# Kernel optimization log

Measured on AMD Instinct MI355X. Metric: run time of the kernel, lower is better.

The kernel has to match this reference:

```python
import jax, jax.numpy as jnp
import numpy as np

B, T, SD = 16, 512, 64          # batch, action seq len, sample_dim
EMB, HD = 1024, 64              # emb_dim, head_dim
NH = EMB // HD                  # 16 heads
DEPTH, NREG, LAT, FF = 8, 16, 256, 4 * EMB
S = T + NREG                    # total sequence length (actions + registers)


def setup_inputs() -> dict:
    key = jax.random.key(0)
    ks = jax.random.split(key, 16)
    def n(k, shape, scale=0.02):
        return jax.random.normal(k, shape, jnp.float32) * scale
    return {
        "sample": jax.random.normal(ks[0], (B, T, SD), jnp.float32),
        "W_emb": n(ks[1], (SD, EMB)), "b_emb": jnp.zeros((EMB,), jnp.float32),
        "pos": n(ks[2], (T, EMB)),
        "registers": n(ks[3], (NREG, EMB), 1.0),
        "ln1_s": jnp.ones((DEPTH, EMB), jnp.float32), "ln1_b": jnp.zeros((DEPTH, EMB), jnp.float32),
        "W_qkv": n(ks[4], (DEPTH, EMB, 3 * EMB)), "b_qkv": jnp.zeros((DEPTH, 3 * EMB), jnp.float32),
        "W_o": n(ks[5], (DEPTH, EMB, EMB)), "b_o": jnp.zeros((DEPTH, EMB), jnp.float32),
        "ln2_s": jnp.ones((DEPTH, EMB), jnp.float32), "ln2_b": jnp.zeros((DEPTH, EMB), jnp.float32),
        "W_fc1": n(ks[6], (DEPTH, EMB, FF)), "b_fc1": jnp.zeros((DEPTH, FF), jnp.float32),
        "W_fc2": n(ks[7], (DEPTH, FF, EMB)), "b_fc2": jnp.zeros((DEPTH, EMB), jnp.float32),
        "lnf_s": jnp.ones((EMB,), jnp.float32), "lnf_b": jnp.zeros((EMB,), jnp.float32),
        "W_head": n(ks[8], (EMB, LAT)), "b_head": jnp.zeros((LAT,), jnp.float32),
    }


def _ln(x, s, b):
    m = jnp.mean(x, -1, keepdims=True)
    v = jnp.var(x, -1, keepdims=True)
    return (x - m) * jax.lax.rsqrt(v + 1e-5) * s + b


def _causal_last_mask():
    # True = attended to. Actions attend to all actions but NOT registers;
    # registers attend to all actions and causally (incl. self) to registers.
    allowed = jnp.ones((S, S), jnp.bool_)
    allowed = allowed.at[:T, T:].set(False)
    allowed = allowed.at[T:, T:].set(jnp.tril(jnp.ones((NREG, NREG), jnp.bool_)))
    return allowed


def reference(sample, W_emb, b_emb, pos, registers, ln1_s, ln1_b, W_qkv, b_qkv,
              W_o, b_o, ln2_s, ln2_b, W_fc1, b_fc1, W_fc2, b_fc2,
              lnf_s, lnf_b, W_head, b_head):
    # embed + positional add
    x = sample @ W_emb + b_emb + pos[None, :, :]          # [B,T,E]
    # concat registers
    x = jnp.concatenate([x, jnp.broadcast_to(registers, (B, NREG, EMB))], axis=1)  # [B,S,E]
    mask = _causal_last_mask()                             # [S,S]
    scale = 1.0 / jnp.sqrt(jnp.asarray(HD, x.dtype))
    for i in range(DEPTH):
        # pre-LN multi-head attention with structured block mask
        h = _ln(x, ln1_s[i], ln1_b[i])
        qkv = h @ W_qkv[i] + b_qkv[i]
        q, k, v = jnp.split(qkv, 3, axis=-1)
        q = q.reshape(B, S, NH, HD)
        k = k.reshape(B, S, NH, HD)
        v = v.reshape(B, S, NH, HD)
        att = jnp.einsum('bqhd,bkhd->bhqk', q, k) * scale
        att = jnp.where(mask[None, None], att, jnp.finfo(att.dtype).min)
        att = jax.nn.softmax(att, axis=-1)
        o = jnp.einsum('bhqk,bkhd->bqhd', att, v).reshape(B, S, EMB)
        x = x + o @ W_o[i] + b_o[i]
        # pre-LN MLP
        h2 = _ln(x, ln2_s[i], ln2_b[i])
        x = x + jax.nn.gelu(h2 @ W_fc1[i] + b_fc1[i]) @ W_fc2[i] + b_fc2[i]
    x = _ln(x, lnf_s, lnf_b)
    # head applied to register positions only
    return x[:, T:] @ W_head + b_head                      # [B,NREG,LAT]
```

## Files before the change

### kernel.cpp

```cpp
#include <hip/hip_runtime.h>
#include <hip/hip_bf16.h>


typedef unsigned short u16;
typedef __attribute__((ext_vector_type(4))) float f32x4;
typedef __attribute__((ext_vector_type(8))) __bf16 bf16x8;

#define DEV static __device__ __forceinline__

constexpr int Bb = 16, Tt = 512, E = 1024, HD = 64, NHd = 16;
constexpr int DEPTH = 8, NREG = 16, LAT = 256, FF = 4096;
constexpr int S = Tt + NREG;
constexpr int SPAD = 576;
constexpr int MR = Bb * S;
constexpr int ME = Bb * Tt;

DEV u16 f2bf(float f) {
  unsigned u = __builtin_bit_cast(unsigned, f);
  u += 0x7fffu + ((u >> 16) & 1u);
  return (u16)(u >> 16);
}

DEV void gll16(const u16* g, u16* l) {
  __builtin_amdgcn_global_load_lds((const __attribute__((address_space(1))) void*)g,
                                   (__attribute__((address_space(3))) void*)l, 16, 0, 0);
}

enum { M_EMBED, M_QKV, M_OPROJ, M_FC1, M_FC2, M_HEAD };

struct GA {
  const u16* A; const u16* Bt;
  int K, lda, ldb, Nrows, ldc;
  const float* bias; const float* pos;
  float* fout; u16* bout;
  u16 *qp, *kp, *vtp;
};

template<int MODE, int BN>
__global__ __launch_bounds__(256)
void gemm_bt(GA g) {
  constexpr int NI = BN / 32;
  __shared__ __align__(16) u16 As[3][128 * 32];
  __shared__ __align__(16) u16 Bs[3][BN * 32];
  const int tid = threadIdx.x;
  const u16* A  = g.A;
  const u16* Bt = g.Bt;

  int tM, tN;
  {
    const int nwg = gridDim.x * gridDim.y;
    int flat = blockIdx.y * gridDim.x + blockIdx.x;
    const int q = nwg >> 3, r = nwg & 7;
    const int xcd = flat & 7, loc = flat >> 3;
    flat = (xcd < r ? xcd * (q + 1) : r * (q + 1) + (xcd - r) * q) + loc;
    tM = flat / gridDim.x; tN = flat % gridDim.x;
  }

  const int lane = tid & 63, wid = tid >> 6;
  const int wr = wid >> 1, wc = wid & 1;
  const int fr = lane & 15, fg = lane >> 4;

  const int arow = tM * 128 + (tid >> 2);
  int br0 = tN * BN + (tid >> 2);
  if (br0 > g.Nrows - 1) br0 = g.Nrows - 1;
  int br1 = tN * BN + 64 + (tid >> 2);
  if (br1 > g.Nrows - 1) br1 = g.Nrows - 1;
  const int kseg = ((tid & 3) ^ ((tid >> 3) & 3)) * 8;
  const int woff = (tid & 192) * 8;

  const u16* ag0 = A  + (long)arow        * g.lda + kseg;
  const u16* ag1 = A  + (long)(arow + 64) * g.lda + kseg;
  const u16* bg0 = Bt + (long)br0         * g.ldb + kseg;
  const u16* bg1 = Bt + (long)br1         * g.ldb + kseg;

  f32x4 acc[4][NI];
#pragma unroll
  for (int i = 0; i < 4; ++i)
#pragma unroll
    for (int j = 0; j < NI; ++j) acc[i][j] = f32x4{0.f, 0.f, 0.f, 0.f};

#define STAGE(KT, BUF) do {                                   \
    const int _k0 = (KT) << 5;                                \
    gll16(ag0 + _k0, &As[BUF][woff]);                         \
    gll16(ag1 + _k0, &As[BUF][woff + 2048]);                  \
    gll16(bg0 + _k0, &Bs[BUF][woff]);                         \
    if (BN == 128) gll16(bg1 + _k0, &Bs[BUF][woff + 2048]);   \
  } while (0)

  const int nk = g.K >> 5;
  STAGE(0, 0);
  if (nk > 1) STAGE(1, 1);

  const int rsw = (fg ^ ((fr >> 1) & 3)) * 8;
  constexpr int LPS = (BN == 128) ? 4 : 3;

  for (int kt = 0; kt < nk; ++kt) {
    const int cur = kt % 3;
    if (kt < nk - 1) {
      asm volatile("s_waitcnt vmcnt(%0)" :: "i"(LPS) : "memory");
    } else {
      asm volatile("s_waitcnt vmcnt(0)" ::: "memory");
    }
    __builtin_amdgcn_sched_barrier(0);
    __builtin_amdgcn_s_barrier();
    __builtin_amdgcn_sched_barrier(0);
    if (kt + 2 < nk) STAGE(kt + 2, (kt + 2) % 3);

    bf16x8 af[4], bfr[NI];
#pragma unroll
    for (int mi = 0; mi < 4; ++mi)
      af[mi] = *(const bf16x8*)&As[cur][(wr * 64 + mi * 16 + fr) * 32 + rsw];
#pragma unroll
    for (int ni = 0; ni < NI; ++ni)
      bfr[ni] = *(const bf16x8*)&Bs[cur][(wc * (BN / 2) + ni * 16 + fr) * 32 + rsw];
    __builtin_amdgcn_s_setprio(1);
#pragma unroll
    for (int mi = 0; mi < 4; ++mi)
#pragma unroll
      for (int ni = 0; ni < NI; ++ni)
        acc[mi][ni] = __builtin_amdgcn_mfma_f32_16x16x32_bf16(af[mi], bfr[ni], acc[mi][ni], 0, 0, 0);
    __builtin_amdgcn_s_setprio(0);
  }
#undef STAGE

#pragma unroll
  for (int mi = 0; mi < 4; ++mi)
#pragma unroll
    for (int ni = 0; ni < NI; ++ni)
#pragma unroll
      for (int j = 0; j < 4; ++j) {
        const int row = tM * 128 + wr * 64 + mi * 16 + fg * 4 + j;
        const int col = tN * BN + wc * (BN / 2) + ni * 16 + fr;
        float v = acc[mi][ni][j];
        if (MODE == M_EMBED) {
          const int b = row >> 9, t = row & 511;
          v += g.bias[col] + g.pos[(long)t * E + col];
          g.fout[((long)(b * S + t)) * E + col] = v;
        } else if (MODE == M_QKV) {
          const int b = row / S, s = row - b * S;
          v += g.bias[col];
          const int part = col >> 10, c = col & 1023;
          const int hh = c >> 6, d = c & 63;
          const u16 bf = f2bf(v);
          if (part == 0)      g.qp [((long)((b * NHd + hh) * SPAD + s)) * HD + d] = bf;
          else if (part == 1) g.kp [((long)((b * NHd + hh) * SPAD + s)) * HD + d] = bf;
          else                g.vtp[((long)((b * NHd + hh) * HD   + d)) * SPAD + s] = bf;
        } else if (MODE == M_OPROJ || MODE == M_FC2) {
          const long idx = (long)row * g.ldc + col;
          g.fout[idx] += v + g.bias[col];
        } else if (MODE == M_FC1) {
          v += g.bias[col];
          const float z = 0.7978845608028654f * (v + 0.044715f * v * v * v);
          const float e = __expf(2.f * z);
          const float th = 1.f - 2.f / (e + 1.f);
          g.bout[(long)row * g.ldc + col] = f2bf(0.5f * v * (1.f + th));
        } else if (MODE == M_HEAD) {
          g.fout[(long)row * g.ldc + col] = v + g.bias[col];
        }
      }
}

__global__ __launch_bounds__(256)
void flash_k(const u16* __restrict__ q, const u16* __restrict__ k,
             const u16* __restrict__ vt, u16* __restrict__ o) {
  __shared__ __align__(16) u16 Ks[2][64 * 64];
  __shared__ __align__(16) u16 Vs[2][64 * 64];
  __shared__ __align__(16) u16 Ps[4 * 16 * 64];
  const int tid = threadIdx.x;
  const int lane = tid & 63, w = tid >> 6;
  const int fr = lane & 15, fg = lane >> 4;

  int flat = blockIdx.y * 9 + blockIdx.x;
  flat = (flat & 7) * 288 + (flat >> 3);
  const int bh = flat / 9, qt = flat % 9;
  const int q0 = qt * 64;

  const u16* qrow = q + ((long)bh * SPAD + q0 + w * 16 + fr) * HD;
  const bf16x8 qf0 = *(const bf16x8*)(qrow + fg * 8);
  const bf16x8 qf1 = *(const bf16x8*)(qrow + 32 + fg * 8);

  const int srow = lane >> 3;
  const int sseg = (((lane & 7) ^ (srow & 7)) * 8);
  const u16* kg = k  + ((long)bh * SPAD + w * 16 + srow) * HD + sseg;
  const u16* vg = vt + ((long)(bh * HD + w * 16 + srow)) * SPAD + sseg;

#define STAGE_F(KT, BUF) do {                                       \
    gll16(kg + (KT) * 64 * HD,          &Ks[BUF][w * 16 * HD]);     \
    gll16(kg + (KT) * 64 * HD + 8 * HD, &Ks[BUF][w * 16 * HD + 8 * HD]); \
    gll16(vg + (KT) * 64,               &Vs[BUF][w * 16 * HD]);     \
    gll16(vg + (KT) * 64 + 8 * SPAD,    &Vs[BUF][w * 16 * HD + 8 * HD]); \
  } while (0)

  const int frm = fr & 7;

  float m[4], lsum[4]; f32x4 oa[4];
#pragma unroll
  for (int j = 0; j < 4; ++j) { m[j] = -1e30f; lsum[j] = 0.f; }
#pragma unroll
  for (int n = 0; n < 4; ++n) oa[n] = f32x4{0.f, 0.f, 0.f, 0.f};

  const int nt = (q0 < Tt) ? 8 : 9;
  STAGE_F(0, 0);
  for (int kt = 0; kt < nt; ++kt) {
    const int cur = kt & 1;
    asm volatile("s_waitcnt vmcnt(0)" ::: "memory");
    __builtin_amdgcn_sched_barrier(0);
    __builtin_amdgcn_s_barrier();
    __builtin_amdgcn_sched_barrier(0);
    if (kt + 1 < nt) STAGE_F(kt + 1, cur ^ 1);

    f32x4 sfr[4];
#pragma unroll
    for (int n = 0; n < 4; ++n) {
      const bf16x8 kf0 = *(const bf16x8*)&Ks[cur][(n * 16 + fr) * HD + ((fg ^ frm) * 8)];
      const bf16x8 kf1 = *(const bf16x8*)&Ks[cur][(n * 16 + fr) * HD + (((fg + 4) ^ frm) * 8)];
      sfr[n] = __builtin_amdgcn_mfma_f32_16x16x32_bf16(qf0, kf0, f32x4{0.f,0.f,0.f,0.f}, 0, 0, 0);
      sfr[n] = __builtin_amdgcn_mfma_f32_16x16x32_bf16(qf1, kf1, sfr[n], 0, 0, 0);
    }
    float p[4][4];
#pragma unroll
    for (int j = 0; j < 4; ++j) {
      const int qg = q0 + w * 16 + fg * 4 + j;
      const int vlim = qg < Tt ? Tt : qg + 1;
#pragma unroll
      for (int n = 0; n < 4; ++n) {
        const int col = kt * 64 + n * 16 + fr;
        p[n][j] = (col < vlim) ? sfr[n][j] * 0.125f : -1e30f;
      }
    }
#pragma unroll
    for (int j = 0; j < 4; ++j) {
      float pm = fmaxf(fmaxf(p[0][j], p[1][j]), fmaxf(p[2][j], p[3][j]));
#pragma unroll
      for (int msk = 1; msk <= 8; msk <<= 1) pm = fmaxf(pm, __shfl_xor(pm, msk));
      const float mn = fmaxf(m[j], pm);
      const float corr = __expf(m[j] - mn);
      m[j] = mn;
      float rs = 0.f;
#pragma unroll
      for (int n = 0; n < 4; ++n) { const float e = __expf(p[n][j] - mn); p[n][j] = e; rs += e; }
#pragma unroll
      for (int msk = 1; msk <= 8; msk <<= 1) rs += __shfl_xor(rs, msk);
      lsum[j] = lsum[j] * corr + rs;
#pragma unroll
      for (int n = 0; n < 4; ++n) oa[n][j] *= corr;
    }
#pragma unroll
    for (int j = 0; j < 4; ++j) {
      const int r = fg * 4 + j;
#pragma unroll
      for (int n = 0; n < 4; ++n) {
        const int gr = 2 * n + (fr >> 3);
        Ps[w * 1024 + r * 64 + ((gr ^ (r & 7)) * 8) + frm] = f2bf(p[n][j]);
      }
    }
    asm volatile("s_waitcnt lgkmcnt(0)" ::: "memory");
    __builtin_amdgcn_sched_barrier(0);
    const bf16x8 pf0 = *(const bf16x8*)&Ps[w * 1024 + fr * 64 + ((fg ^ frm) * 8)];
    const bf16x8 pf1 = *(const bf16x8*)&Ps[w * 1024 + fr * 64 + (((fg + 4) ^ frm) * 8)];
#pragma unroll
    for (int n = 0; n < 4; ++n) {
      const bf16x8 vf0 = *(const bf16x8*)&Vs[cur][(n * 16 + fr) * HD + ((fg ^ frm) * 8)];
      const bf16x8 vf1 = *(const bf16x8*)&Vs[cur][(n * 16 + fr) * HD + (((fg + 4) ^ frm) * 8)];
      oa[n] = __builtin_amdgcn_mfma_f32_16x16x32_bf16(pf0, vf0, oa[n], 0, 0, 0);
      oa[n] = __builtin_amdgcn_mfma_f32_16x16x32_bf16(pf1, vf1, oa[n], 0, 0, 0);
    }
  }
#undef STAGE_F

  const int b = bh >> 4, hh = bh & 15;
#pragma unroll
  for (int j = 0; j < 4; ++j) {
    const int qg = q0 + w * 16 + fg * 4 + j;
    if (qg < S) {
      const float inv = 1.f / lsum[j];
#pragma unroll
      for (int n = 0; n < 4; ++n)
        o[((long)(b * S + qg)) * E + hh * HD + n * 16 + fr] = f2bf(oa[n][j] * inv);
    }
  }
}

__global__ __launch_bounds__(256)
void ln_k(const float* __restrict__ x, const float* __restrict__ sc,
          const float* __restrict__ bi, u16* __restrict__ out, int gather) {
  const int r = blockIdx.x;
  const int srow = gather ? ((r >> 4) * S + Tt + (r & 15)) : r;
  const float4 v = ((const float4*)(x + (long)srow * E))[threadIdx.x];
  float s = v.x + v.y + v.z + v.w;
  float q = v.x * v.x + v.y * v.y + v.z * v.z + v.w * v.w;
#pragma unroll
  for (int o = 32; o; o >>= 1) { s += __shfl_down(s, o); q += __shfl_down(q, o); }
  __shared__ float ps[8];
  if ((threadIdx.x & 63) == 0) { ps[threadIdx.x >> 6] = s; ps[4 + (threadIdx.x >> 6)] = q; }
  __syncthreads();
  s = ps[0] + ps[1] + ps[2] + ps[3];
  q = ps[4] + ps[5] + ps[6] + ps[7];
  const float mean = s * (1.f / E);
  const float rs = rsqrtf(q * (1.f / E) - mean * mean + 1e-5f);
  const int c = threadIdx.x * 4;
  ushort4 o4;
  o4.x = f2bf((v.x - mean) * rs * sc[c + 0] + bi[c + 0]);
  o4.y = f2bf((v.y - mean) * rs * sc[c + 1] + bi[c + 1]);
  o4.z = f2bf((v.z - mean) * rs * sc[c + 2] + bi[c + 2]);
  o4.w = f2bf((v.w - mean) * rs * sc[c + 3] + bi[c + 3]);
  ((ushort4*)(out + (long)r * E))[threadIdx.x] = o4;
}

__global__ __launch_bounds__(256)
void wtrans(const float* __restrict__ src, u16* __restrict__ dst, int R, int C) {
  __shared__ float t[32][33];
  const int c0 = blockIdx.x * 32, r0 = blockIdx.y * 32;
  const int tx = threadIdx.x & 31, ty = threadIdx.x >> 5;
#pragma unroll
  for (int i = 0; i < 32; i += 8) t[ty + i][tx] = src[(long)(r0 + ty + i) * C + c0 + tx];
  __syncthreads();
#pragma unroll
  for (int i = 0; i < 32; i += 8) dst[(long)(c0 + ty + i) * R + r0 + tx] = f2bf(t[tx][ty + i]);
}

__global__ void cvt_bf(const float* __restrict__ in, u16* __restrict__ out, long n) {
  const long i = ((long)blockIdx.x * blockDim.x + threadIdx.x) * 4;
  if (i >= n) return;
  const float4 v = *(const float4*)(in + i);
  ushort4 o; o.x = f2bf(v.x); o.y = f2bf(v.y); o.z = f2bf(v.z); o.w = f2bf(v.w);
  *(ushort4*)(out + i) = o;
}

__global__ void zero_k(float4* p, long n) {
  long i = (long)blockIdx.x * blockDim.x + threadIdx.x;
  const long st = (long)gridDim.x * blockDim.x;
  const float4 z = make_float4(0.f, 0.f, 0.f, 0.f);
  for (; i < n; i += st) p[i] = z;
}

__global__ void reg_copy(const float* __restrict__ regs, float* __restrict__ x) {
  const int b = blockIdx.x >> 4, r = blockIdx.x & 15;
  const float4* sp = (const float4*)(regs + (long)r * E);
  float4* dp = (float4*)(x + ((long)(b * S + Tt + r)) * E);
  dp[threadIdx.x] = sp[threadIdx.x];
}

constexpr long OFF_WQKV = 0L;
constexpr long OFF_WO   = OFF_WQKV + 3072L * 1024 * 2;
constexpr long OFF_WFC1 = OFF_WO   + 1024L * 1024 * 2;
constexpr long OFF_WFC2 = OFF_WFC1 + 4096L * 1024 * 2;
constexpr long OFF_WEMB = OFF_WFC2 + 1024L * 4096 * 2;
constexpr long OFF_WHEAD= OFF_WEMB + 1024L * 64 * 2;
constexpr long OFF_SMP  = OFF_WHEAD+ 256L * 1024 * 2;
constexpr long OFF_X    = OFF_SMP  + (long)ME * 64 * 2;
constexpr long OFF_H    = OFF_X    + (long)MR * E * 4;
constexpr long OFF_Q    = OFF_H    + (long)MR * E * 2;
constexpr long OFF_K    = OFF_Q    + 256L * SPAD * HD * 2;
constexpr long OFF_VT   = OFF_K    + 256L * SPAD * HD * 2;
constexpr long OFF_O    = OFF_VT   + 256L * SPAD * HD * 2;
constexpr long OFF_HF   = OFF_O    + (long)MR * FF * 2;
constexpr long WS_NEED  = OFF_HF   + 256L * 1024 * 2;

extern "C" void kernel_launch(void* const* d_in, const int* in_sizes, int n_in,
                              void* d_out, int out_size, void* d_ws, size_t ws_size,
                              hipStream_t stream) {
  if (ws_size < (size_t)WS_NEED) return;

  const float* sample = (const float*)d_in[0];
  const float* W_emb  = (const float*)d_in[1];
  const float* b_emb  = (const float*)d_in[2];
  const float* pos    = (const float*)d_in[3];
  const float* regs   = (const float*)d_in[4];
  const float* ln1_s  = (const float*)d_in[5];
  const float* ln1_b  = (const float*)d_in[6];
  const float* W_qkv  = (const float*)d_in[7];
  const float* b_qkv  = (const float*)d_in[8];
  const float* W_o    = (const float*)d_in[9];
  const float* b_o    = (const float*)d_in[10];
  const float* ln2_s  = (const float*)d_in[11];
  const float* ln2_b  = (const float*)d_in[12];
  const float* W_fc1  = (const float*)d_in[13];
  const float* b_fc1  = (const float*)d_in[14];
  const float* W_fc2  = (const float*)d_in[15];
  const float* b_fc2  = (const float*)d_in[16];
  const float* lnf_s  = (const float*)d_in[17];
  const float* lnf_b  = (const float*)d_in[18];
  const float* W_head = (const float*)d_in[19];
  const float* b_head = (const float*)d_in[20];

  char* w = (char*)d_ws;
  u16* wqkvT = (u16*)(w + OFF_WQKV);
  u16* woT   = (u16*)(w + OFF_WO);
  u16* wfc1T = (u16*)(w + OFF_WFC1);
  u16* wfc2T = (u16*)(w + OFF_WFC2);
  u16* wembT = (u16*)(w + OFF_WEMB);
  u16* wheadT= (u16*)(w + OFF_WHEAD);
  u16* smp   = (u16*)(w + OFF_SMP);
  float* x   = (float*)(w + OFF_X);
  u16* h     = (u16*)(w + OFF_H);
  u16* qp    = (u16*)(w + OFF_Q);
  u16* kp    = (u16*)(w + OFF_K);
  u16* vtp   = (u16*)(w + OFF_VT);
  u16* o     = (u16*)(w + OFF_O);
  u16* a1    = (u16*)(w + OFF_O);
  u16* hf    = (u16*)(w + OFF_HF);

  wtrans<<<dim3(32, 2, 1), 256, 0, stream>>>(W_emb,  wembT, 64, 1024);
  wtrans<<<dim3(8, 32, 1), 256, 0, stream>>>(W_head, wheadT, 1024, 256);
  cvt_bf<<<dim3(512), 256, 0, stream>>>(sample, smp, (long)ME * 64);
  zero_k<<<dim3(2048), 256, 0, stream>>>((float4*)qp, (3L * 256 * SPAD * HD * 2) / 16);

  {
    GA g{}; g.A = smp; g.Bt = wembT; g.K = 64; g.lda = 64; g.ldb = 64;
    g.Nrows = E; g.bias = b_emb; g.pos = pos; g.fout = x;
    gemm_bt<M_EMBED, 64><<<dim3(16, 64, 1), 256, 0, stream>>>(g);
  }
  reg_copy<<<dim3(256), 256, 0, stream>>>(regs, x);

  for (int L = 0; L < DEPTH; ++L) {
    wtrans<<<dim3(96, 32, 1),  256, 0, stream>>>(W_qkv + (long)L * 1024 * 3072, wqkvT, 1024, 3072);
    wtrans<<<dim3(32, 32, 1),  256, 0, stream>>>(W_o   + (long)L * 1024 * 1024, woT,   1024, 1024);
    wtrans<<<dim3(128, 32, 1), 256, 0, stream>>>(W_fc1 + (long)L * 1024 * 4096, wfc1T, 1024, 4096);
    wtrans<<<dim3(32, 128, 1), 256, 0, stream>>>(W_fc2 + (long)L * 4096 * 1024, wfc2T, 4096, 1024);

    ln_k<<<dim3(MR), 256, 0, stream>>>(x, ln1_s + L * E, ln1_b + L * E, h, 0);
    {
      GA g{}; g.A = h; g.Bt = wqkvT;
      g.K = 1024; g.lda = 1024; g.ldb = 1024; g.Nrows = 3072;
      g.bias = b_qkv + L * 3072; g.qp = qp; g.kp = kp; g.vtp = vtp;
      gemm_bt<M_QKV, 128><<<dim3(24, 66, 1), 256, 0, stream>>>(g);
    }
    flash_k<<<dim3(9, 256, 1), 256, 0, stream>>>(qp, kp, vtp, o);
    {
      GA g{}; g.A = o; g.Bt = woT;
      g.K = 1024; g.lda = 1024; g.ldb = 1024; g.Nrows = 1024; g.ldc = 1024;
      g.bias = b_o + L * E; g.fout = x;
      gemm_bt<M_OPROJ, 64><<<dim3(16, 66, 1), 256, 0, stream>>>(g);
    }
    ln_k<<<dim3(MR), 256, 0, stream>>>(x, ln2_s + L * E, ln2_b + L * E, h, 0);
    {
      GA g{}; g.A = h; g.Bt = wfc1T;
      g.K = 1024; g.lda = 1024; g.ldb = 1024; g.Nrows = 4096; g.ldc = 4096;
      g.bias = b_fc1 + L * FF; g.bout = a1;
      gemm_bt<M_FC1, 128><<<dim3(32, 66, 1), 256, 0, stream>>>(g);
    }
    {
      GA g{}; g.A = a1; g.Bt = wfc2T;
      g.K = 4096; g.lda = 4096; g.ldb = 4096; g.Nrows = 1024; g.ldc = 1024;
      g.bias = b_fc2 + L * E; g.fout = x;
      gemm_bt<M_FC2, 64><<<dim3(16, 66, 1), 256, 0, stream>>>(g);
    }
  }

  ln_k<<<dim3(256), 256, 0, stream>>>(x, lnf_s, lnf_b, hf, 1);
  {
    GA g{}; g.A = hf; g.Bt = wheadT; g.K = 1024; g.lda = 1024; g.ldb = 1024;
    g.Nrows = LAT; g.ldc = LAT; g.bias = b_head; g.fout = (float*)d_out;
    gemm_bt<M_HEAD, 128><<<dim3(2, 2, 1), 256, 0, stream>>>(g);
  }
}
```

Before: 4.307 ms.

## Enlarge flash query tile, fuse weight transposes, widen GEMM N tiles

The flash attention kernel now gives each wave 32 query rows (128 per block), so every K/V tile loaded into LDS is reused across twice as many queries. The grid drops from 9 to 5 query tiles per head, and the last tile's out-of-range Q rows are clamped. The four per-layer weight transpose launches are merged into one kernel that picks its source matrix from the block index, removing launch overhead. The O-projection and FC2 GEMMs move to a 128-wide N tile with half the blocks in N. This raises register pressure in flash and lowers GEMM block count, which may reduce occupancy or load balance.

Result: faster. 3.886 ms (-9.8%).

```diff
diff --git a/kernel.cpp b/kernel.cpp
--- a/kernel.cpp
+++ b/kernel.cpp
@@ -20,6 +20,7 @@
   u += 0x7fffu + ((u >> 16) & 1u);
   return (u16)(u >> 16);
 }
+DEV float bf2f(u16 h) { return __builtin_bit_cast(float, (unsigned)h << 16); }
 
 DEV void gll16(const u16* g, u16* l) {
   __builtin_amdgcn_global_load_lds((const __attribute__((address_space(1))) void*)g,
@@ -165,19 +166,25 @@
              const u16* __restrict__ vt, u16* __restrict__ o) {
   __shared__ __align__(16) u16 Ks[2][64 * 64];
   __shared__ __align__(16) u16 Vs[2][64 * 64];
-  __shared__ __align__(16) u16 Ps[4 * 16 * 64];
+  __shared__ __align__(16) u16 Ps[4 * 32 * 64];
   const int tid = threadIdx.x;
   const int lane = tid & 63, w = tid >> 6;
   const int fr = lane & 15, fg = lane >> 4;
 
-  int flat = blockIdx.y * 9 + blockIdx.x;
-  flat = (flat & 7) * 288 + (flat >> 3);
-  const int bh = flat / 9, qt = flat % 9;
-  const int q0 = qt * 64;
-
-  const u16* qrow = q + ((long)bh * SPAD + q0 + w * 16 + fr) * HD;
-  const bf16x8 qf0 = *(const bf16x8*)(qrow + fg * 8);
-  const bf16x8 qf1 = *(const bf16x8*)(qrow + 32 + fg * 8);
+  int flat = blockIdx.y * 5 + blockIdx.x;
+  flat = (flat & 7) * 160 + (flat >> 3);
+  const int bh = flat / 5, qt = flat % 5;
+  const int q0 = qt * 128;
+
+  bf16x8 qf[2][2];
+#pragma unroll
+  for (int ms = 0; ms < 2; ++ms) {
+    int qr = q0 + w * 32 + ms * 16 + fr;
+    if (qr > SPAD - 1) qr = SPAD - 1;
+    const u16* qrow = q + ((long)bh * SPAD + qr) * HD;
+    qf[ms][0] = *(const bf16x8*)(qrow + fg * 8);
+    qf[ms][1] = *(const bf16x8*)(qrow + 32 + fg * 8);
+  }
 
   const int srow = lane >> 3;
   const int sseg = (((lane & 7) ^ (srow & 7)) * 8);
@@ -193,13 +200,17 @@
 
   const int frm = fr & 7;
 
-  float m[4], lsum[4]; f32x4 oa[4];
-#pragma unroll
-  for (int j = 0; j < 4; ++j) { m[j] = -1e30f; lsum[j] = 0.f; }
-#pragma unroll
-  for (int n = 0; n < 4; ++n) oa[n] = f32x4{0.f, 0.f, 0.f, 0.f};
-
-  const int nt = (q0 < Tt) ? 8 : 9;
+  float m[2][4], lsum[2][4]; f32x4 oa[2][4];
+#pragma unroll
+  for (int ms = 0; ms < 2; ++ms)
+#pragma unroll
+    for (int j = 0; j < 4; ++j) { m[ms][j] = -1e30f; lsum[ms][j] = 0.f; }
+#pragma unroll
+  for (int ms = 0; ms < 2; ++ms)
+#pragma unroll
+    for (int n = 0; n < 4; ++n) oa[ms][n] = f32x4{0.f, 0.f, 0.f, 0.f};
+
+  const int nt = (qt < 4) ? 8 : 9;
   STAGE_F(0, 0);
   for (int kt = 0; kt < nt; ++kt) {
     const int cur = kt & 1;
@@ -209,76 +220,94 @@
     __builtin_amdgcn_sched_barrier(0);
     if (kt + 1 < nt) STAGE_F(kt + 1, cur ^ 1);
 
-    f32x4 sfr[4];
+    f32x4 sfr[2][4];
 #pragma unroll
     for (int n = 0; n < 4; ++n) {
       const bf16x8 kf0 = *(const bf16x8*)&Ks[cur][(n * 16 + fr) * HD + ((fg ^ frm) * 8)];
       const bf16x8 kf1 = *(const bf16x8*)&Ks[cur][(n * 16 + fr) * HD + (((fg + 4) ^ frm) * 8)];
-      sfr[n] = __builtin_amdgcn_mfma_f32_16x16x32_bf16(qf0, kf0, f32x4{0.f,0.f,0.f,0.f}, 0, 0, 0);
-      sfr[n] = __builtin_amdgcn_mfma_f32_16x16x32_bf16(qf1, kf1, sfr[n], 0, 0, 0);
-    }
-    float p[4][4];
-#pragma unroll
-    for (int j = 0; j < 4; ++j) {
-      const int qg = q0 + w * 16 + fg * 4 + j;
-      const int vlim = qg < Tt ? Tt : qg + 1;
-#pragma unroll
-      for (int n = 0; n < 4; ++n) {
-        const int col = kt * 64 + n * 16 + fr;
-        p[n][j] = (col < vlim) ? sfr[n][j] * 0.125f : -1e30f;
-      }
-    }
-#pragma unroll
-    for (int j = 0; j < 4; ++j) {
-      float pm = fmaxf(fmaxf(p[0][j], p[1][j]), fmaxf(p[2][j], p[3][j]));
-#pragma unroll
-      for (int msk = 1; msk <= 8; msk <<= 1) pm = fmaxf(pm, __shfl_xor(pm, msk));
-      const float mn = fmaxf(m[j], pm);
-      const float corr = __expf(m[j] - mn);
-      m[j] = mn;
-      float rs = 0.f;
-#pragma unroll
-      for (int n = 0; n < 4; ++n) { const float e = __expf(p[n][j] - mn); p[n][j] = e; rs += e; }
-#pragma unroll
-      for (int msk = 1; msk <= 8; msk <<= 1) rs += __shfl_xor(rs, msk);
-      lsum[j] = lsum[j] * corr + rs;
-#pragma unroll
-      for (int n = 0; n < 4; ++n) oa[n][j] *= corr;
-    }
-#pragma unroll
-    for (int j = 0; j < 4; ++j) {
-      const int r = fg * 4 + j;
-#pragma unroll
-      for (int n = 0; n < 4; ++n) {
-        const int gr = 2 * n + (fr >> 3);
-        Ps[w * 1024 + r * 64 + ((gr ^ (r & 7)) * 8) + frm] = f2bf(p[n][j]);
-      }
-    }
+#pragma unroll
+      for (int ms = 0; ms < 2; ++ms) {
+        sfr[ms][n] = __builtin_amdgcn_mfma_f32_16x16x32_bf16(qf[ms][0], kf0, f32x4{0.f,0.f,0.f,0.f}, 0, 0, 0);
+        sfr[ms][n] = __builtin_amdgcn_mfma_f32_16x16x32_bf16(qf[ms][1], kf1, sfr[ms][n], 0, 0, 0);
+      }
+    }
+    float p[2][4][4];
+#pragma unroll
+    for (int ms = 0; ms < 2; ++ms)
+#pragma unroll
+      for (int j = 0; j < 4; ++j) {
+        const int qg = q0 + w * 32 + ms * 16 + fg * 4 + j;
+        const int vlim = qg < Tt ? Tt : qg + 1;
+#pragma unroll
+        for (int n = 0; n < 4; ++n) {
+          const int col = kt * 64 + n * 16 + fr;
+          p[ms][n][j] = (col < vlim) ? sfr[ms][n][j] * 0.125f : -1e30f;
+        }
+      }
+#pragma unroll
+    for (int ms = 0; ms < 2; ++ms)
+#pragma unroll
+      for (int j = 0; j < 4; ++j) {
+        float pm = fmaxf(fmaxf(p[ms][0][j], p[ms][1][j]), fmaxf(p[ms][2][j], p[ms][3][j]));
+#pragma unroll
+        for (int msk = 1; msk <= 8; msk <<= 1) pm = fmaxf(pm, __shfl_xor(pm, msk));
+        const float mn = fmaxf(m[ms][j], pm);
+        const float corr = __expf(m[ms][j] - mn);
+        m[ms][j] = mn;
+        float rs = 0.f;
+#pragma unroll
+        for (int n = 0; n < 4; ++n) { const float e = __expf(p[ms][n][j] - mn); p[ms][n][j] = e; rs += e; }
+#pragma unroll
+        for (int msk = 1; msk <= 8; msk <<= 1) rs += __shfl_xor(rs, msk);
+        lsum[ms][j] = lsum[ms][j] * corr + rs;
+#pragma unroll
+        for (int n = 0; n < 4; ++n) oa[ms][n][j] *= corr;
+      }
+#pragma unroll
+    for (int ms = 0; ms < 2; ++ms)
+#pragma unroll
+      for (int j = 0; j < 4; ++j) {
+        const int r = ms * 16 + fg * 4 + j;
+#pragma unroll
+        for (int n = 0; n < 4; ++n) {
+          const int gr = 2 * n + (fr >> 3);
+          Ps[w * 2048 + r * 64 + ((gr ^ (r & 7)) * 8) + frm] = f2bf(p[ms][n][j]);
+        }
+      }
     asm volatile("s_waitcnt lgkmcnt(0)" ::: "memory");
     __builtin_amdgcn_sched_barrier(0);
-    const bf16x8 pf0 = *(const bf16x8*)&Ps[w * 1024 + fr * 64 + ((fg ^ frm) * 8)];
-    const bf16x8 pf1 = *(const bf16x8*)&Ps[w * 1024 + fr * 64 + (((fg + 4) ^ frm) * 8)];
+    bf16x8 pf[2][2];
+#pragma unroll
+    for (int ms = 0; ms < 2; ++ms) {
+      pf[ms][0] = *(const bf16x8*)&Ps[w * 2048 + (ms * 16 + fr) * 64 + ((fg ^ frm) * 8)];
+      pf[ms][1] = *(const bf16x8*)&Ps[w * 2048 + (ms * 16 + fr) * 64 + (((fg + 4) ^ frm) * 8)];
+    }
 #pragma unroll
     for (int n = 0; n < 4; ++n) {
       const bf16x8 vf0 = *(const bf16x8*)&Vs[cur][(n * 16 + fr) * HD + ((fg ^ frm) * 8)];
       const bf16x8 vf1 = *(const bf16x8*)&Vs[cur][(n * 16 + fr) * HD + (((fg + 4) ^ frm) * 8)];
-      oa[n] = __builtin_amdgcn_mfma_f32_16x16x32_bf16(pf0, vf0, oa[n], 0, 0, 0);
-      oa[n] = __builtin_amdgcn_mfma_f32_16x16x32_bf16(pf1, vf1, oa[n], 0, 0, 0);
+#pragma unroll
+      for (int ms = 0; ms < 2; ++ms) {
+        oa[ms][n] = __builtin_amdgcn_mfma_f32_16x16x32_bf16(pf[ms][0], vf0, oa[ms][n], 0, 0, 0);
+        oa[ms][n] = __builtin_amdgcn_mfma_f32_16x16x32_bf16(pf[ms][1], vf1, oa[ms][n], 0, 0, 0);
+      }
     }
   }
 #undef STAGE_F
 
   const int b = bh >> 4, hh = bh & 15;
 #pragma unroll
-  for (int j = 0; j < 4; ++j) {
-    const int qg = q0 + w * 16 + fg * 4 + j;
-    if (qg < S) {
-      const float inv = 1.f / lsum[j];
-#pragma unroll
-      for (int n = 0; n < 4; ++n)
-        o[((long)(b * S + qg)) * E + hh * HD + n * 16 + fr] = f2bf(oa[n][j] * inv);
-    }
-  }
+  for (int ms = 0; ms < 2; ++ms)
+#pragma unroll
+    for (int j = 0; j < 4; ++j) {
+      const int qg = q0 + w * 32 + ms * 16 + fg * 4 + j;
+      if (qg < S) {
+        const float inv = 1.f / lsum[ms][j];
+#pragma unroll
+        for (int n = 0; n < 4; ++n)
+          o[((long)(b * S + qg)) * E + hh * HD + n * 16 + fr] = f2bf(oa[ms][n][j] * inv);
+      }
+    }
 }
 
 __global__ __launch_bounds__(256)
@@ -317,6 +346,27 @@
   __syncthreads();
 #pragma unroll
   for (int i = 0; i < 32; i += 8) dst[(long)(c0 + ty + i) * R + r0 + tx] = f2bf(t[tx][ty + i]);
+}
+
+struct WT4 {
+  const float* s[4]; u16* d[4];
+  int R[4], C[4], tx[4], st[4];
+};
+__global__ __launch_bounds__(256)
+void wtrans4(WT4 a) {
+  const int bid = blockIdx.x;
+  const int wsel = (bid >= a.st[1]) + (bid >= a.st[2]) + (bid >= a.st[3]);
+  const int t = bid - a.st[wsel];
+  const int c0 = (t % a.tx[wsel]) * 32, r0 = (t / a.tx[wsel]) * 32;
+  const float* src = a.s[wsel]; u16* dst = a.d[wsel];
+  const int R = a.R[wsel], C = a.C[wsel];
+  __shared__ float tt[32][33];
+  const int tx = threadIdx.x & 31, ty = threadIdx.x >> 5;
+#pragma unroll
+  for (int i = 0; i < 32; i += 8) tt[ty + i][tx] = src[(long)(r0 + ty + i) * C + c0 + tx];
+  __syncthreads();
+#pragma unroll
+  for (int i = 0; i < 32; i += 8) dst[(long)(c0 + ty + i) * R + r0 + tx] = f2bf(tt[tx][ty + i]);
 }
 
 __global__ void cvt_bf(const float* __restrict__ in, u16* __restrict__ out, long n) {
@@ -414,10 +464,14 @@
   reg_copy<<<dim3(256), 256, 0, stream>>>(regs, x);
 
   for (int L = 0; L < DEPTH; ++L) {
-    wtrans<<<dim3(96, 32, 1),  256, 0, stream>>>(W_qkv + (long)L * 1024 * 3072, wqkvT, 1024, 3072);
-    wtrans<<<dim3(32, 32, 1),  256, 0, stream>>>(W_o   + (long)L * 1024 * 1024, woT,   1024, 1024);
-    wtrans<<<dim3(128, 32, 1), 256, 0, stream>>>(W_fc1 + (long)L * 1024 * 4096, wfc1T, 1024, 4096);
-    wtrans<<<dim3(32, 128, 1), 256, 0, stream>>>(W_fc2 + (long)L * 4096 * 1024, wfc2T, 4096, 1024);
+    {
+      WT4 a;
+      a.s[0] = W_qkv + (long)L * 1024 * 3072; a.d[0] = wqkvT; a.R[0] = 1024; a.C[0] = 3072; a.tx[0] = 96;  a.st[0] = 0;
+      a.s[1] = W_o   + (long)L * 1024 * 1024; a.d[1] = woT;   a.R[1] = 1024; a.C[1] = 1024; a.tx[1] = 32;  a.st[1] = 3072;
+      a.s[2] = W_fc1 + (long)L * 1024 * 4096; a.d[2] = wfc1T; a.R[2] = 1024; a.C[2] = 4096; a.tx[2] = 128; a.st[2] = 4096;
+      a.s[3] = W_fc2 + (long)L * 4096 * 1024; a.d[3] = wfc2T; a.R[3] = 4096; a.C[3] = 1024; a.tx[3] = 32;  a.st[3] = 8192;
+      wtrans4<<<dim3(12288), 256, 0, stream>>>(a);
+    }
 
     ln_k<<<dim3(MR), 256, 0, stream>>>(x, ln1_s + L * E, ln1_b + L * E, h, 0);
     {
@@ -426,12 +480,12 @@
       g.bias = b_qkv + L * 3072; g.qp = qp; g.kp = kp; g.vtp = vtp;
       gemm_bt<M_QKV, 128><<<dim3(24, 66, 1), 256, 0, stream>>>(g);
     }
-    flash_k<<<dim3(9, 256, 1), 256, 0, stream>>>(qp, kp, vtp, o);
+    flash_k<<<dim3(5, 256, 1), 256, 0, stream>>>(qp, kp, vtp, o);
     {
       GA g{}; g.A = o; g.Bt = woT;
       g.K = 1024; g.lda = 1024; g.ldb = 1024; g.Nrows = 1024; g.ldc = 1024;
       g.bias = b_o + L * E; g.fout = x;
-      gemm_bt<M_OPROJ, 64><<<dim3(16, 66, 1), 256, 0, stream>>>(g);
+      gemm_bt<M_OPROJ, 128><<<dim3(8, 66, 1), 256, 0, stream>>>(g);
     }
     ln_k<<<dim3(MR), 256, 0, stream>>>(x, ln2_s + L * E, ln2_b + L * E, h, 0);
     {
@@ -444,7 +498,7 @@
       GA g{}; g.A = a1; g.Bt = wfc2T;
       g.K = 4096; g.lda = 4096; g.ldb = 4096; g.Nrows = 1024; g.ldc = 1024;
       g.bias = b_fc2 + L * E; g.fout = x;
-      gemm_bt<M_FC2, 64><<<dim3(16, 66, 1), 256, 0, stream>>>(g);
+      gemm_bt<M_FC2, 128><<<dim3(8, 66, 1), 256, 0, stream>>>(g);
     }
   }
 
```
